# Optimization experiments

Hardware: AMD Instinct MI355X
Metric: run time of the kernel (lower is better)

Reference implementation:

```python
import jax, jax.numpy as jnp
import numpy as np

D_MODEL = 1024
H = 16
D_K = D_MODEL // H
B, S = 1, 4096


def setup_inputs() -> dict:
    key = jax.random.key(0)
    ks = jax.random.split(key, 12)
    std = 1.0 / np.sqrt(D_MODEL)
    inp = {
        "q": jax.random.normal(ks[0], (B, S, D_MODEL), dtype=jnp.float32),
        "k": jax.random.normal(ks[1], (B, S, D_MODEL), dtype=jnp.float32),
        "v": jax.random.normal(ks[2], (B, S, D_MODEL), dtype=jnp.float32),
        "mask": jax.random.randint(ks[3], (B, 1, S, S), 0, 2).astype(bool),
        # nn.Linear params (torch convention: y = x @ W.T + b), weights [out, in]
        "wq": jax.random.uniform(ks[4], (D_MODEL, D_MODEL), jnp.float32, -std, std),
        "bq": jax.random.uniform(ks[5], (D_MODEL,), jnp.float32, -std, std),
        "wk": jax.random.uniform(ks[6], (D_MODEL, D_MODEL), jnp.float32, -std, std),
        "bk": jax.random.uniform(ks[7], (D_MODEL,), jnp.float32, -std, std),
        "wv": jax.random.uniform(ks[8], (D_MODEL, D_MODEL), jnp.float32, -std, std),
        "bv": jax.random.uniform(ks[9], (D_MODEL,), jnp.float32, -std, std),
        "wo": jax.random.uniform(ks[10], (D_MODEL, D_MODEL), jnp.float32, -std, std),
        "bo": jax.random.uniform(ks[11], (D_MODEL,), jnp.float32, -std, std),
    }
    return inp


def _split_heads(x):
    # [b, s, (h d)] -> [b, h, s, d]
    b, s, _ = x.shape
    return x.reshape(b, s, H, D_K).transpose(0, 2, 1, 3)


def reference(q, k, v, mask, wq, bq, wk, bk, wv, bv, wo, bo):
    b, s, d = q.shape
    qh = _split_heads(q @ wq.T + bq)
    kh = _split_heads(k @ wk.T + bk)
    vh = _split_heads(v @ wv.T + bv)
    # NOTE: original scales by sqrt(d_model), not sqrt(d_k) — keep faithful.
    score = jnp.einsum("bhqd,bhkd->bhqk", qh, kh) / jnp.sqrt(jnp.float32(d))
    score = jnp.where(mask, jnp.float32(-1e9), score)
    attn = jax.nn.softmax(score, axis=-1)  # dropout is identity in eval mode
    wv_out = jnp.einsum("bhqk,bhkd->bhqd", attn, vh)
    concat = wv_out.transpose(0, 2, 1, 3).reshape(b, s, d)
    return concat @ wo.T + bo
```

## Files before the change

kernel.cpp:

```cpp
#include <hip/hip_runtime.h>
#include <hip/hip_bf16.h>
#include <math.h>

typedef __attribute__((ext_vector_type(4))) float f32x4;
typedef __attribute__((ext_vector_type(8))) short s16x8;
typedef __attribute__((ext_vector_type(4))) short s16x4;

#define S_LEN 4096
#define DMODEL 1024
#define NHEADS 16
#define DHEAD 64

__device__ __forceinline__ unsigned short f2bf(float f) {
  union { float f; unsigned int u; } x; x.f = f;
  return (unsigned short)((x.u + 0x7FFFu + ((x.u >> 16) & 1u)) >> 16);
}

__device__ __forceinline__ void gload_lds16(const void* g, void* l) {
  __builtin_amdgcn_global_load_lds(
      (const __attribute__((address_space(1))) unsigned int*)g,
      (__attribute__((address_space(3))) unsigned int*)l, 16, 0, 0);
}

__global__ __launch_bounds__(256) void mask_pack(const int* __restrict__ mask,
                                                 unsigned long long* __restrict__ bits) {
  const int qr = blockIdx.x;
  const int wv = threadIdx.x >> 6, l = threadIdx.x & 63;
  const int* row = mask + (size_t)qr * S_LEN;
#pragma unroll
  for (int w0 = 0; w0 < 64; w0 += 4) {
    const int w = w0 + wv;
    unsigned long long b = __ballot(row[w * 64 + l] != 0);
    if (l == 0) bits[(size_t)qr * 64 + w] = b;
  }
}

__global__ __launch_bounds__(256) void cast_bf16(
    const float* __restrict__ s0, const float* __restrict__ s1, const float* __restrict__ s2,
    const float* __restrict__ s3, const float* __restrict__ s4, const float* __restrict__ s5,
    const float* __restrict__ s6, unsigned short* __restrict__ dst) {
  const int z = blockIdx.y;
  const float* src = (z == 0) ? s0 : (z == 1) ? s1 : (z == 2) ? s2 :
                     (z == 3) ? s3 : (z == 4) ? s4 : (z == 5) ? s5 : s6;
  const int n = (z < 3) ? (S_LEN * DMODEL) : (DMODEL * DMODEL);
  unsigned short* d = dst + ((z < 3) ? (size_t)z * S_LEN * DMODEL
                                     : (size_t)3 * S_LEN * DMODEL + (size_t)(z - 3) * DMODEL * DMODEL);
  const int i = (blockIdx.x * 256 + threadIdx.x) * 4;
  if (i < n) {
    f32x4 v = *(const f32x4*)(src + i);
    s16x4 o;
#pragma unroll
    for (int j = 0; j < 4; ++j) o[j] = (short)f2bf(v[j]);
    *(s16x4*)(d + i) = o;
  }
}

template<int A_BF16, int B_BF16, int OUT_MODE>
__device__ __forceinline__ void gemm_body(const void* __restrict__ Ap,
                                          const void* __restrict__ Wp,
                                          const float* __restrict__ bias,
                                          void* __restrict__ outp, float scale) {
  constexpr int K = DMODEL, N = DMODEL, M = S_LEN;
  constexpr int BM = 128, BK = 32, LDT = 40;
  __shared__ unsigned short Alds[BM * LDT];
  __shared__ unsigned short Blds[BM * LDT];
  const int tid = threadIdx.x;
  const int l = tid & 63, wid = tid >> 6;
  const int lr = l & 15, lg = l >> 4;
  const int bm = blockIdx.x * BM;
  const int bn = blockIdx.y * BM;
  const int wm = (wid >> 1) * 64, wn = (wid & 1) * 64;

  f32x4 acc[4][4] = {};

  for (int k0 = 0; k0 < K; k0 += BK) {
    __syncthreads();
    if constexpr (A_BF16) {
      const unsigned short* A = (const unsigned short*)Ap;
      const int col = (tid & 3) * 8, row = tid >> 2;
#pragma unroll
      for (int p = 0; p < 2; ++p) {
        const int r = row + p * 64;
        *(s16x8*)&Alds[r * LDT + col] =
            *(const s16x8*)(A + (size_t)(bm + r) * K + k0 + col);
      }
    } else {
      const float* A = (const float*)Ap;
      const int col = (tid & 7) * 4, row = tid >> 3;
#pragma unroll
      for (int p = 0; p < 4; ++p) {
        const int r = row + p * 32;
        f32x4 vv = *(const f32x4*)(A + (size_t)(bm + r) * K + k0 + col);
        s16x4 o;
#pragma unroll
        for (int j = 0; j < 4; ++j) o[j] = (short)f2bf(vv[j]);
        *(s16x4*)&Alds[r * LDT + col] = o;
      }
    }
    if constexpr (B_BF16) {
      const unsigned short* W = (const unsigned short*)Wp;
      const int col = (tid & 3) * 8, row = tid >> 2;
#pragma unroll
      for (int p = 0; p < 2; ++p) {
        const int r = row + p * 64;
        *(s16x8*)&Blds[r * LDT + col] =
            *(const s16x8*)(W + (size_t)(bn + r) * K + k0 + col);
      }
    } else {
      const float* W = (const float*)Wp;
      const int col = (tid & 7) * 4, row = tid >> 3;
#pragma unroll
      for (int p = 0; p < 4; ++p) {
        const int r = row + p * 32;
        f32x4 vv = *(const f32x4*)(W + (size_t)(bn + r) * K + k0 + col);
        s16x4 o;
#pragma unroll
        for (int j = 0; j < 4; ++j) o[j] = (short)f2bf(vv[j]);
        *(s16x4*)&Blds[r * LDT + col] = o;
      }
    }
    __syncthreads();
    s16x8 af[4], bfr[4];
#pragma unroll
    for (int mi = 0; mi < 4; ++mi)
      af[mi] = *(const s16x8*)&Alds[(wm + mi * 16 + lr) * LDT + lg * 8];
#pragma unroll
    for (int ni = 0; ni < 4; ++ni)
      bfr[ni] = *(const s16x8*)&Blds[(wn + ni * 16 + lr) * LDT + lg * 8];
#pragma unroll
    for (int mi = 0; mi < 4; ++mi)
#pragma unroll
      for (int ni = 0; ni < 4; ++ni)
        acc[mi][ni] = __builtin_amdgcn_mfma_f32_16x16x32_bf16(af[mi], bfr[ni], acc[mi][ni], 0, 0, 0);
  }

#pragma unroll
  for (int ni = 0; ni < 4; ++ni) {
    const int n = bn + wn + ni * 16 + lr;
    const float bv = bias[n];
#pragma unroll
    for (int mi = 0; mi < 4; ++mi) {
#pragma unroll
      for (int j = 0; j < 4; ++j) {
        const int m = bm + wm + mi * 16 + lg * 4 + j;
        const float val = (acc[mi][ni][j] + bv) * scale;
        if constexpr (OUT_MODE == 1) {
          unsigned short* out = (unsigned short*)outp;
          out[((size_t)(n >> 6) * M + m) * DHEAD + (n & 63)] = f2bf(val);
        } else if constexpr (OUT_MODE == 2) {
          unsigned short* out = (unsigned short*)outp;
          out[((size_t)(n >> 6) * DHEAD + (n & 63)) * M + m] = f2bf(val);
        } else {
          float* out = (float*)outp;
          out[(size_t)m * N + n] = val;
        }
      }
    }
  }
}

__global__ __launch_bounds__(256) void proj_qk_f32(
    const float* __restrict__ q, const float* __restrict__ k,
    const float* __restrict__ wq, const float* __restrict__ bq,
    const float* __restrict__ wk, const float* __restrict__ bk,
    unsigned short* __restrict__ ws) {
  const int z = blockIdx.z;
  gemm_body<0, 0, 1>((z == 0) ? q : k, (z == 0) ? wq : wk, (z == 0) ? bq : bk,
                     ws + (size_t)z * S_LEN * DMODEL, (z == 0) ? 0.03125f : 1.0f);
}
__global__ __launch_bounds__(256) void proj_v_f32(
    const float* __restrict__ v, const float* __restrict__ wv,
    const float* __restrict__ bv, unsigned short* __restrict__ out) {
  gemm_body<0, 0, 2>(v, wv, bv, out, 1.0f);
}
__global__ __launch_bounds__(256) void outproj_f32(
    const unsigned short* __restrict__ concat, const float* __restrict__ wo,
    const float* __restrict__ bo, float* __restrict__ out) {
  gemm_body<1, 0, 0>(concat, wo, bo, out, 1.0f);
}

__global__ __launch_bounds__(256) void proj_qk_b16(
    const unsigned short* __restrict__ qb, const unsigned short* __restrict__ kb,
    const unsigned short* __restrict__ wqb, const float* __restrict__ bq,
    const unsigned short* __restrict__ wkb, const float* __restrict__ bk,
    unsigned short* __restrict__ ws) {
  const int z = blockIdx.z;
  gemm_body<1, 1, 1>((z == 0) ? qb : kb, (z == 0) ? wqb : wkb, (z == 0) ? bq : bk,
                     ws + (size_t)z * S_LEN * DMODEL, (z == 0) ? 0.03125f : 1.0f);
}
__global__ __launch_bounds__(256) void proj_v_b16(
    const unsigned short* __restrict__ vb, const unsigned short* __restrict__ wvb,
    const float* __restrict__ bv, unsigned short* __restrict__ out) {
  gemm_body<1, 1, 2>(vb, wvb, bv, out, 1.0f);
}
__global__ __launch_bounds__(256) void outproj_b16(
    const unsigned short* __restrict__ concat, const unsigned short* __restrict__ wob,
    const float* __restrict__ bo, float* __restrict__ out) {
  gemm_body<1, 1, 0>(concat, wob, bo, out, 1.0f);
}

__global__ __launch_bounds__(512, 4) void attn_fwd(
    const unsigned short* __restrict__ Qh, const unsigned short* __restrict__ Kh,
    const unsigned short* __restrict__ Vt, const unsigned long long* __restrict__ bits,
    unsigned short* __restrict__ concat) {
  __shared__ unsigned short Klds[2][64 * 64];
  __shared__ unsigned short Vlds[2][64 * 64];
  __shared__ unsigned short P_lds[8][16][72];

  const int tid = threadIdx.x;
  const int l = tid & 63, wid = tid >> 6;
  const int lr = l & 15, lg = l >> 4;
  const int swz = (blockIdx.x & 7) * 64 + (blockIdx.x >> 3);
  const int h = swz >> 5;
  const int qrow0 = (swz & 31) * 128 + wid * 16;

  const unsigned short* Qbase = Qh + ((size_t)h * S_LEN + qrow0) * DHEAD;
  s16x8 qf[2];
#pragma unroll
  for (int ds = 0; ds < 2; ++ds)
    qf[ds] = *(const s16x8*)(Qbase + lr * DHEAD + ds * 32 + lg * 8);

  const unsigned short* Kbase = Kh + (size_t)h * S_LEN * DHEAD;
  const unsigned short* Vbase = Vt + (size_t)h * DHEAD * S_LEN;
  const unsigned long long* mrow = bits + (size_t)(qrow0 + lr) * 64;

  const int srow = l >> 3;
  const int schunk = (l & 7) ^ srow;
  const unsigned short* Kst = Kbase + (size_t)(wid * 8 + srow) * DHEAD + schunk * 8;
  const unsigned short* Vst = Vbase + (size_t)(wid * 8 + srow) * S_LEN + schunk * 8;
  const int sdst = (wid * 8) * 64;

  f32x4 o_acc[4] = {};
  float lsum = 0.f;

  gload_lds16(Kst, &Klds[0][sdst]);
  gload_lds16(Vst, &Vlds[0][sdst]);
  __syncthreads();

  const int xr = lr & 7;

  for (int t = 0; t < 64; ++t) {
    const int buf = t & 1;
    if (t < 63) {
      gload_lds16(Kst + (size_t)(t + 1) * 64 * DHEAD, &Klds[buf ^ 1][sdst]);
      gload_lds16(Vst + (t + 1) * 64, &Vlds[buf ^ 1][sdst]);
    }

    const unsigned long long mw = mrow[t];

    const unsigned short* Kb = &Klds[buf][0];
    s16x8 kf[8];
#pragma unroll
    for (int kg = 0; kg < 4; ++kg) {
      const int r = kg * 16 + lr;
      kf[kg * 2]     = *(const s16x8*)(Kb + r * 64 + ((lg ^ xr) * 8));
      kf[kg * 2 + 1] = *(const s16x8*)(Kb + r * 64 + (((lg + 4) ^ xr) * 8));
    }
    f32x4 sc[4];
    __builtin_amdgcn_s_setprio(1);
#pragma unroll
    for (int kg = 0; kg < 4; ++kg) {
      f32x4 z = {};
      z = __builtin_amdgcn_mfma_f32_16x16x32_bf16(kf[kg * 2], qf[0], z, 0, 0, 0);
      sc[kg] = __builtin_amdgcn_mfma_f32_16x16x32_bf16(kf[kg * 2 + 1], qf[1], z, 0, 0, 0);
    }
    __builtin_amdgcn_s_setprio(0);

    const unsigned short* Vb = &Vlds[buf][0];
    s16x8 vf[8];
#pragma unroll
    for (int dg = 0; dg < 4; ++dg) {
      const int r = dg * 16 + lr;
      vf[dg * 2]     = *(const s16x8*)(Vb + r * 64 + ((lg ^ xr) * 8));
      vf[dg * 2 + 1] = *(const s16x8*)(Vb + r * 64 + (((lg + 4) ^ xr) * 8));
    }

#pragma unroll
    for (int kg = 0; kg < 4; ++kg) {
      const unsigned int part = (unsigned int)(mw >> (kg * 16 + lg * 4));
#pragma unroll
      for (int j = 0; j < 4; ++j) {
        const float sv = ((part >> j) & 1u) ? -1e9f : sc[kg][j];
        const float p = __expf(sv);
        sc[kg][j] = p;
        lsum += p;
      }
    }

#pragma unroll
    for (int kg = 0; kg < 4; ++kg) {
#pragma unroll
      for (int w = 0; w < 2; ++w) {
        unsigned int pk;
        asm("v_cvt_pk_bf16_f32 %0, %1, %2"
            : "=v"(pk) : "v"(sc[kg][2 * w]), "v"(sc[kg][2 * w + 1]));
        *(unsigned int*)&P_lds[wid][lr][kg * 16 + lg * 4 + 2 * w] = pk;
      }
    }

    s16x8 pf[2];
#pragma unroll
    for (int ks = 0; ks < 2; ++ks)
      pf[ks] = *(const s16x8*)&P_lds[wid][lr][ks * 32 + lg * 8];

    __builtin_amdgcn_s_setprio(1);
#pragma unroll
    for (int dg = 0; dg < 4; ++dg)
#pragma unroll
      for (int ks = 0; ks < 2; ++ks)
        o_acc[dg] = __builtin_amdgcn_mfma_f32_16x16x32_bf16(pf[ks], vf[dg * 2 + ks], o_acc[dg], 0, 0, 0);
    __builtin_amdgcn_s_setprio(0);

    __syncthreads();
  }

  lsum += __shfl_xor(lsum, 16, 64);
  lsum += __shfl_xor(lsum, 32, 64);
  float rs[4];
#pragma unroll
  for (int j = 0; j < 4; ++j) rs[j] = __shfl(lsum, lg * 4 + j, 64);

#pragma unroll
  for (int dg = 0; dg < 4; ++dg)
#pragma unroll
    for (int j = 0; j < 4; ++j) {
      const int qr = qrow0 + lg * 4 + j;
      const int d = dg * 16 + lr;
      concat[(size_t)qr * DMODEL + h * DHEAD + d] = f2bf(o_acc[dg][j] / rs[j]);
    }
}

extern "C" void kernel_launch(void* const* d_in, const int* in_sizes, int n_in,
                              void* d_out, int out_size, void* d_ws, size_t ws_size,
                              hipStream_t stream) {
  const float* q  = (const float*)d_in[0];
  const float* k  = (const float*)d_in[1];
  const float* v  = (const float*)d_in[2];
  const int* mask = (const int*)d_in[3];
  const float* wq = (const float*)d_in[4];
  const float* bq = (const float*)d_in[5];
  const float* wk = (const float*)d_in[6];
  const float* bk = (const float*)d_in[7];
  const float* wv = (const float*)d_in[8];
  const float* bv = (const float*)d_in[9];
  const float* wo = (const float*)d_in[10];
  const float* bo = (const float*)d_in[11];
  float* out = (float*)d_out;

  unsigned short* wsq = (unsigned short*)d_ws;
  unsigned short* wsk = wsq + (size_t)S_LEN * DMODEL;
  unsigned short* wsv = wsk + (size_t)S_LEN * DMODEL;
  unsigned short* wsc = wsv + (size_t)S_LEN * DMODEL;
  unsigned long long* wsbits = (unsigned long long*)(wsc + (size_t)S_LEN * DMODEL);
  unsigned short* cast0 = (unsigned short*)(wsbits + (size_t)S_LEN * 64);
  const size_t need = (size_t)((char*)(cast0 + 3 * (size_t)S_LEN * DMODEL
                                       + 4 * (size_t)DMODEL * DMODEL) - (char*)d_ws);
  const bool big = ws_size >= need;

  mask_pack<<<dim3(S_LEN), dim3(256), 0, stream>>>(mask, wsbits);

  if (big) {
    unsigned short* qb  = cast0;
    unsigned short* kb  = qb + (size_t)S_LEN * DMODEL;
    unsigned short* vb  = kb + (size_t)S_LEN * DMODEL;
    unsigned short* wqb = vb + (size_t)S_LEN * DMODEL;
    unsigned short* wkb = wqb + (size_t)DMODEL * DMODEL;
    unsigned short* wvb = wkb + (size_t)DMODEL * DMODEL;
    unsigned short* wob = wvb + (size_t)DMODEL * DMODEL;
    cast_bf16<<<dim3(4096, 7), dim3(256), 0, stream>>>(q, k, v, wq, wk, wv, wo, qb);
    proj_qk_b16<<<dim3(32, 8, 2), dim3(256), 0, stream>>>(qb, kb, wqb, bq, wkb, bk, wsq);
    proj_v_b16<<<dim3(32, 8), dim3(256), 0, stream>>>(vb, wvb, bv, wsv);
    attn_fwd<<<dim3(512), dim3(512), 0, stream>>>(wsq, wsk, wsv, wsbits, wsc);
    outproj_b16<<<dim3(32, 8), dim3(256), 0, stream>>>(wsc, wob, bo, out);
  } else {
    proj_qk_f32<<<dim3(32, 8, 2), dim3(256), 0, stream>>>(q, k, wq, bq, wk, bk, wsq);
    proj_v_f32<<<dim3(32, 8), dim3(256), 0, stream>>>(v, wv, bv, wsv);
    attn_fwd<<<dim3(512), dim3(512), 0, stream>>>(wsq, wsk, wsv, wsbits, wsc);
    outproj_f32<<<dim3(32, 8), dim3(256), 0, stream>>>(wsc, wo, bo, out);
  }
}
```

Before: 224.7 us.

## Split KV across blocks, double per-wave query rows, and transpose mask to SGPR layout

The attention kernel now processes 32 query rows per wave, so each K/V LDS fragment feeds twice as many MFMAs, and splits the KV range in two across blocks to keep the grid at 512 blocks. A separate combine kernel merges the unnormalised bf16 partial outputs with their row sums. The mask is pre-transposed into per-lane 64-bit words so masking becomes a v_cndmask with an SGPR operand, and exp uses exp2 with log2(e) folded into the Q scale. The Q/K/V projections are merged into one launch. Costs are an extra transpose kernel, a combine kernel, partial-output traffic, and bf16 rounding of the partials before they are combined.

```diff
diff --git a/kernel.cpp b/kernel.cpp
--- a/kernel.cpp
+++ b/kernel.cpp
@@ -14,6 +14,14 @@
 __device__ __forceinline__ unsigned short f2bf(float f) {
   union { float f; unsigned int u; } x; x.f = f;
   return (unsigned short)((x.u + 0x7FFFu + ((x.u >> 16) & 1u)) >> 16);
+}
+
+__device__ __forceinline__ float fexp2(float x) {
+#if __has_builtin(__builtin_amdgcn_exp2f)
+  return __builtin_amdgcn_exp2f(x);
+#else
+  float r; asm("v_exp_f32 %0, %1" : "=v"(r) : "v"(x)); return r;
+#endif
 }
 
 __device__ __forceinline__ void gload_lds16(const void* g, void* l) {
@@ -33,6 +41,22 @@
     unsigned long long b = __ballot(row[w * 64 + l] != 0);
     if (l == 0) bits[(size_t)qr * 64 + w] = b;
   }
+}
+
+__global__ __launch_bounds__(256) void mask_xpose(const unsigned long long* __restrict__ bits,
+                                                  unsigned long long* __restrict__ lmask) {
+  const int wv = blockIdx.x * 4 + (threadIdx.x >> 6);
+  const int l = threadIdx.x & 63, lr = l & 15, lg4 = (l >> 4) * 4;
+  const int qg = wv >> 6, t = wv & 63;
+  const unsigned long long rw = bits[(size_t)(qg * 16 + lr) * 64 + t];
+  unsigned long long mine = 0;
+#pragma unroll
+  for (int w = 0; w < 16; ++w) {
+    const int sh = (w >> 2) * 16 + (w & 3) + lg4;
+    unsigned long long b = __ballot(((rw >> sh) & 1ull) != 0);
+    if (l == w) mine = b;
+  }
+  if (l < 16) lmask[((size_t)qg * 64 + t) * 16 + l] = mine;
 }
 
 __global__ __launch_bounds__(256) void cast_bf16(
@@ -159,19 +183,35 @@
   }
 }
 
-__global__ __launch_bounds__(256) void proj_qk_f32(
-    const float* __restrict__ q, const float* __restrict__ k,
+#define QSCALE 0.04508422f
+
+__global__ __launch_bounds__(256) void proj_qkv_b16(
+    const unsigned short* __restrict__ qb, const unsigned short* __restrict__ kb,
+    const unsigned short* __restrict__ vb,
+    const unsigned short* __restrict__ wqb, const float* __restrict__ bq,
+    const unsigned short* __restrict__ wkb, const float* __restrict__ bk,
+    const unsigned short* __restrict__ wvb, const float* __restrict__ bv,
+    unsigned short* __restrict__ ws) {
+  const int z = blockIdx.z;
+  if (z == 0)      gemm_body<1, 1, 1>(qb, wqb, bq, ws, QSCALE);
+  else if (z == 1) gemm_body<1, 1, 1>(kb, wkb, bk, ws + (size_t)S_LEN * DMODEL, 1.0f);
+  else             gemm_body<1, 1, 2>(vb, wvb, bv, ws + (size_t)2 * S_LEN * DMODEL, 1.0f);
+}
+__global__ __launch_bounds__(256) void proj_qkv_f32(
+    const float* __restrict__ q, const float* __restrict__ k, const float* __restrict__ v,
     const float* __restrict__ wq, const float* __restrict__ bq,
     const float* __restrict__ wk, const float* __restrict__ bk,
+    const float* __restrict__ wv, const float* __restrict__ bv,
     unsigned short* __restrict__ ws) {
   const int z = blockIdx.z;
-  gemm_body<0, 0, 1>((z == 0) ? q : k, (z == 0) ? wq : wk, (z == 0) ? bq : bk,
-                     ws + (size_t)z * S_LEN * DMODEL, (z == 0) ? 0.03125f : 1.0f);
-}
-__global__ __launch_bounds__(256) void proj_v_f32(
-    const float* __restrict__ v, const float* __restrict__ wv,
-    const float* __restrict__ bv, unsigned short* __restrict__ out) {
-  gemm_body<0, 0, 2>(v, wv, bv, out, 1.0f);
+  if (z == 0)      gemm_body<0, 0, 1>(q, wq, bq, ws, QSCALE);
+  else if (z == 1) gemm_body<0, 0, 1>(k, wk, bk, ws + (size_t)S_LEN * DMODEL, 1.0f);
+  else             gemm_body<0, 0, 2>(v, wv, bv, ws + (size_t)2 * S_LEN * DMODEL, 1.0f);
+}
+__global__ __launch_bounds__(256) void outproj_b16(
+    const unsigned short* __restrict__ concat, const unsigned short* __restrict__ wob,
+    const float* __restrict__ bo, float* __restrict__ out) {
+  gemm_body<1, 1, 0>(concat, wob, bo, out, 1.0f);
 }
 __global__ __launch_bounds__(256) void outproj_f32(
     const unsigned short* __restrict__ concat, const float* __restrict__ wo,
@@ -179,59 +219,52 @@
   gemm_body<1, 0, 0>(concat, wo, bo, out, 1.0f);
 }
 
-__global__ __launch_bounds__(256) void proj_qk_b16(
-    const unsigned short* __restrict__ qb, const unsigned short* __restrict__ kb,
-    const unsigned short* __restrict__ wqb, const float* __restrict__ bq,
-    const unsigned short* __restrict__ wkb, const float* __restrict__ bk,
-    unsigned short* __restrict__ ws) {
-  const int z = blockIdx.z;
-  gemm_body<1, 1, 1>((z == 0) ? qb : kb, (z == 0) ? wqb : wkb, (z == 0) ? bq : bk,
-                     ws + (size_t)z * S_LEN * DMODEL, (z == 0) ? 0.03125f : 1.0f);
-}
-__global__ __launch_bounds__(256) void proj_v_b16(
-    const unsigned short* __restrict__ vb, const unsigned short* __restrict__ wvb,
-    const float* __restrict__ bv, unsigned short* __restrict__ out) {
-  gemm_body<1, 1, 2>(vb, wvb, bv, out, 1.0f);
-}
-__global__ __launch_bounds__(256) void outproj_b16(
-    const unsigned short* __restrict__ concat, const unsigned short* __restrict__ wob,
-    const float* __restrict__ bo, float* __restrict__ out) {
-  gemm_body<1, 1, 0>(concat, wob, bo, out, 1.0f);
-}
-
+template<int NSPLIT>
 __global__ __launch_bounds__(512, 4) void attn_fwd(
     const unsigned short* __restrict__ Qh, const unsigned short* __restrict__ Kh,
-    const unsigned short* __restrict__ Vt, const unsigned long long* __restrict__ bits,
-    unsigned short* __restrict__ concat) {
+    const unsigned short* __restrict__ Vt, const unsigned long long* __restrict__ lmask,
+    unsigned short* __restrict__ outp,
+    float* __restrict__ lpart) {
   __shared__ unsigned short Klds[2][64 * 64];
   __shared__ unsigned short Vlds[2][64 * 64];
-  __shared__ unsigned short P_lds[8][16][72];
+  __shared__ unsigned short P_lds[8][32][72];
 
   const int tid = threadIdx.x;
   const int l = tid & 63, wid = tid >> 6;
   const int lr = l & 15, lg = l >> 4;
-  const int swz = (blockIdx.x & 7) * 64 + (blockIdx.x >> 3);
-  const int h = swz >> 5;
-  const int qrow0 = (swz & 31) * 128 + wid * 16;
+  const int per = 32 * NSPLIT;
+  const int swz = (blockIdx.x & 7) * per + (blockIdx.x >> 3);
+  const int h = swz / (16 * NSPLIT);
+  const int split = (NSPLIT == 2) ? ((swz >> 4) & 1) : 0;
+  const int qb = swz & 15;
+  const int qrow0 = qb * 256 + wid * 32;
+  const int kv0 = split * (S_LEN / NSPLIT);
+  constexpr int NT = (S_LEN / NSPLIT) / 64;
+  const int T0 = kv0 >> 6;
 
   const unsigned short* Qbase = Qh + ((size_t)h * S_LEN + qrow0) * DHEAD;
-  s16x8 qf[2];
-#pragma unroll
-  for (int ds = 0; ds < 2; ++ds)
-    qf[ds] = *(const s16x8*)(Qbase + lr * DHEAD + ds * 32 + lg * 8);
-
-  const unsigned short* Kbase = Kh + (size_t)h * S_LEN * DHEAD;
-  const unsigned short* Vbase = Vt + (size_t)h * DHEAD * S_LEN;
-  const unsigned long long* mrow = bits + (size_t)(qrow0 + lr) * 64;
+  s16x8 qf[2][2];
+#pragma unroll
+  for (int sub = 0; sub < 2; ++sub)
+#pragma unroll
+    for (int ds = 0; ds < 2; ++ds)
+      qf[sub][ds] = *(const s16x8*)(Qbase + (sub * 16 + lr) * DHEAD + ds * 32 + lg * 8);
+
+  const int wid_u = __builtin_amdgcn_readfirstlane(wid);
+  const int qg0 = qb * 16 + wid_u * 2;
+  const unsigned long long* mq0 = lmask + (size_t)qg0 * 64 * 16;
+  const unsigned long long* mq1 = mq0 + (size_t)64 * 16;
 
   const int srow = l >> 3;
   const int schunk = (l & 7) ^ srow;
-  const unsigned short* Kst = Kbase + (size_t)(wid * 8 + srow) * DHEAD + schunk * 8;
-  const unsigned short* Vst = Vbase + (size_t)(wid * 8 + srow) * S_LEN + schunk * 8;
+  const unsigned short* Kst = Kh + (size_t)h * S_LEN * DHEAD
+                              + (size_t)(kv0 + wid * 8 + srow) * DHEAD + schunk * 8;
+  const unsigned short* Vst = Vt + (size_t)h * DHEAD * S_LEN
+                              + (size_t)(wid * 8 + srow) * S_LEN + kv0 + schunk * 8;
   const int sdst = (wid * 8) * 64;
 
-  f32x4 o_acc[4] = {};
-  float lsum = 0.f;
+  f32x4 o_acc[2][4] = {};
+  float lsum[2] = {0.f, 0.f};
 
   gload_lds16(Kst, &Klds[0][sdst]);
   gload_lds16(Vst, &Vlds[0][sdst]);
@@ -239,95 +272,144 @@
 
   const int xr = lr & 7;
 
-  for (int t = 0; t < 64; ++t) {
+  for (int t = 0; t < NT; ++t) {
     const int buf = t & 1;
-    if (t < 63) {
+    if (t < NT - 1) {
       gload_lds16(Kst + (size_t)(t + 1) * 64 * DHEAD, &Klds[buf ^ 1][sdst]);
       gload_lds16(Vst + (t + 1) * 64, &Vlds[buf ^ 1][sdst]);
     }
 
-    const unsigned long long mw = mrow[t];
-
     const unsigned short* Kb = &Klds[buf][0];
-    s16x8 kf[8];
+    f32x4 sc[2][4];
+    __builtin_amdgcn_s_setprio(1);
 #pragma unroll
     for (int kg = 0; kg < 4; ++kg) {
       const int r = kg * 16 + lr;
-      kf[kg * 2]     = *(const s16x8*)(Kb + r * 64 + ((lg ^ xr) * 8));
-      kf[kg * 2 + 1] = *(const s16x8*)(Kb + r * 64 + (((lg + 4) ^ xr) * 8));
-    }
-    f32x4 sc[4];
+      s16x8 k0 = *(const s16x8*)(Kb + r * 64 + ((lg ^ xr) * 8));
+      s16x8 k1 = *(const s16x8*)(Kb + r * 64 + (((lg + 4) ^ xr) * 8));
+#pragma unroll
+      for (int sub = 0; sub < 2; ++sub) {
+        f32x4 z = {};
+        z = __builtin_amdgcn_mfma_f32_16x16x32_bf16(k0, qf[sub][0], z, 0, 0, 0);
+        sc[sub][kg] = __builtin_amdgcn_mfma_f32_16x16x32_bf16(k1, qf[sub][1], z, 0, 0, 0);
+      }
+    }
+    __builtin_amdgcn_s_setprio(0);
+
+    const size_t mo = (size_t)(T0 + t) * 16;
+#pragma unroll
+    for (int sub = 0; sub < 2; ++sub) {
+      const unsigned long long* qp = (sub ? mq1 : mq0) + mo;
+#pragma unroll
+      for (int kg = 0; kg < 4; ++kg) {
+        float p[4];
+#pragma unroll
+        for (int j = 0; j < 4; ++j) {
+          const unsigned long long mw = qp[kg * 4 + j];
+          float pv = fexp2(sc[sub][kg][j]);
+          asm("v_cndmask_b32 %0, %1, 0, %2" : "=v"(pv) : "v"(pv), "s"(mw));
+          p[j] = pv;
+          lsum[sub] += pv;
+        }
+        unsigned int w0, w1;
+        asm("v_cvt_pk_bf16_f32 %0, %1, %2" : "=v"(w0) : "v"(p[0]), "v"(p[1]));
+        asm("v_cvt_pk_bf16_f32 %0, %1, %2" : "=v"(w1) : "v"(p[2]), "v"(p[3]));
+        uint2 pk; pk.x = w0; pk.y = w1;
+        *(uint2*)&P_lds[wid][sub * 16 + lr][kg * 16 + lg * 4] = pk;
+      }
+    }
+    asm volatile("s_waitcnt lgkmcnt(0)" ::: "memory");
+    __builtin_amdgcn_sched_barrier(0);
+
+    s16x8 pf[2][2];
+#pragma unroll
+    for (int sub = 0; sub < 2; ++sub)
+#pragma unroll
+      for (int ks = 0; ks < 2; ++ks)
+        pf[sub][ks] = *(const s16x8*)&P_lds[wid][sub * 16 + lr][ks * 32 + lg * 8];
+
+    const unsigned short* Vb = &Vlds[buf][0];
     __builtin_amdgcn_s_setprio(1);
-#pragma unroll
-    for (int kg = 0; kg < 4; ++kg) {
-      f32x4 z = {};
-      z = __builtin_amdgcn_mfma_f32_16x16x32_bf16(kf[kg * 2], qf[0], z, 0, 0, 0);
-      sc[kg] = __builtin_amdgcn_mfma_f32_16x16x32_bf16(kf[kg * 2 + 1], qf[1], z, 0, 0, 0);
-    }
-    __builtin_amdgcn_s_setprio(0);
-
-    const unsigned short* Vb = &Vlds[buf][0];
-    s16x8 vf[8];
 #pragma unroll
     for (int dg = 0; dg < 4; ++dg) {
       const int r = dg * 16 + lr;
-      vf[dg * 2]     = *(const s16x8*)(Vb + r * 64 + ((lg ^ xr) * 8));
-      vf[dg * 2 + 1] = *(const s16x8*)(Vb + r * 64 + (((lg + 4) ^ xr) * 8));
-    }
-
-#pragma unroll
-    for (int kg = 0; kg < 4; ++kg) {
-      const unsigned int part = (unsigned int)(mw >> (kg * 16 + lg * 4));
-#pragma unroll
-      for (int j = 0; j < 4; ++j) {
-        const float sv = ((part >> j) & 1u) ? -1e9f : sc[kg][j];
-        const float p = __expf(sv);
-        sc[kg][j] = p;
-        lsum += p;
-      }
-    }
-
-#pragma unroll
-    for (int kg = 0; kg < 4; ++kg) {
-#pragma unroll
-      for (int w = 0; w < 2; ++w) {
-        unsigned int pk;
-        asm("v_cvt_pk_bf16_f32 %0, %1, %2"
-            : "=v"(pk) : "v"(sc[kg][2 * w]), "v"(sc[kg][2 * w + 1]));
-        *(unsigned int*)&P_lds[wid][lr][kg * 16 + lg * 4 + 2 * w] = pk;
-      }
-    }
-
-    s16x8 pf[2];
-#pragma unroll
-    for (int ks = 0; ks < 2; ++ks)
-      pf[ks] = *(const s16x8*)&P_lds[wid][lr][ks * 32 + lg * 8];
-
-    __builtin_amdgcn_s_setprio(1);
-#pragma unroll
-    for (int dg = 0; dg < 4; ++dg)
-#pragma unroll
-      for (int ks = 0; ks < 2; ++ks)
-        o_acc[dg] = __builtin_amdgcn_mfma_f32_16x16x32_bf16(pf[ks], vf[dg * 2 + ks], o_acc[dg], 0, 0, 0);
+      s16x8 v0 = *(const s16x8*)(Vb + r * 64 + ((lg ^ xr) * 8));
+      s16x8 v1 = *(const s16x8*)(Vb + r * 64 + (((lg + 4) ^ xr) * 8));
+#pragma unroll
+      for (int sub = 0; sub < 2; ++sub) {
+        o_acc[sub][dg] = __builtin_amdgcn_mfma_f32_16x16x32_bf16(pf[sub][0], v0, o_acc[sub][dg], 0, 0, 0);
+        o_acc[sub][dg] = __builtin_amdgcn_mfma_f32_16x16x32_bf16(pf[sub][1], v1, o_acc[sub][dg], 0, 0, 0);
+      }
+    }
     __builtin_amdgcn_s_setprio(0);
 
     __syncthreads();
   }
 
-  lsum += __shfl_xor(lsum, 16, 64);
-  lsum += __shfl_xor(lsum, 32, 64);
-  float rs[4];
-#pragma unroll
-  for (int j = 0; j < 4; ++j) rs[j] = __shfl(lsum, lg * 4 + j, 64);
-
-#pragma unroll
-  for (int dg = 0; dg < 4; ++dg)
-#pragma unroll
-    for (int j = 0; j < 4; ++j) {
-      const int qr = qrow0 + lg * 4 + j;
-      const int d = dg * 16 + lr;
-      concat[(size_t)qr * DMODEL + h * DHEAD + d] = f2bf(o_acc[dg][j] / rs[j]);
-    }
+#pragma unroll
+  for (int sub = 0; sub < 2; ++sub) {
+    lsum[sub] += __shfl_xor(lsum[sub], 16, 64);
+    lsum[sub] += __shfl_xor(lsum[sub], 32, 64);
+  }
+
+  if constexpr (NSPLIT == 2) {
+    unsigned short* op = outp + ((size_t)(split * NHEADS + h) * S_LEN) * DHEAD;
+#pragma unroll
+    for (int sub = 0; sub < 2; ++sub)
+#pragma unroll
+      for (int dg = 0; dg < 4; ++dg)
+#pragma unroll
+        for (int j = 0; j < 4; ++j) {
+          const int q = qrow0 + sub * 16 + lg * 4 + j;
+          op[(size_t)q * DHEAD + dg * 16 + lr] = f2bf(o_acc[sub][dg][j]);
+        }
+    if (l < 16) {
+      float* lp = lpart + (size_t)(split * NHEADS + h) * S_LEN + qrow0;
+      lp[lr] = lsum[0];
+      lp[16 + lr] = lsum[1];
+    }
+  } else {
+    float rs[2][4];
+#pragma unroll
+    for (int sub = 0; sub < 2; ++sub)
+#pragma unroll
+      for (int j = 0; j < 4; ++j)
+        rs[sub][j] = __shfl(lsum[sub], lg * 4 + j, 64);
+#pragma unroll
+    for (int sub = 0; sub < 2; ++sub)
+#pragma unroll
+      for (int dg = 0; dg < 4; ++dg)
+#pragma unroll
+        for (int j = 0; j < 4; ++j) {
+          const int q = qrow0 + sub * 16 + lg * 4 + j;
+          outp[(size_t)q * DMODEL + h * DHEAD + dg * 16 + lr] =
+              f2bf(o_acc[sub][dg][j] / rs[sub][j]);
+        }
+  }
+}
+
+__global__ __launch_bounds__(256) void attn_combine(
+    const unsigned short* __restrict__ opart, const float* __restrict__ lpart,
+    unsigned short* __restrict__ concat) {
+  const int idx = blockIdx.x * 256 + threadIdx.x;
+  const int d4 = (idx & 15) * 4;
+  const int hq = idx >> 4;
+  const int h = hq >> 12, q = hq & 4095;
+  const size_t o0 = ((size_t)h * S_LEN + q) * DHEAD + d4;
+  const size_t o1 = o0 + (size_t)NHEADS * S_LEN * DHEAD;
+  const float linv = 1.0f / (lpart[(size_t)h * S_LEN + q] +
+                             lpart[(size_t)(NHEADS + h) * S_LEN + q]);
+  s16x4 a = *(const s16x4*)(opart + o0);
+  s16x4 b = *(const s16x4*)(opart + o1);
+  s16x4 r;
+#pragma unroll
+  for (int i = 0; i < 4; ++i) {
+    union { unsigned int u; float f; } xa, xb;
+    xa.u = ((unsigned int)(unsigned short)a[i]) << 16;
+    xb.u = ((unsigned int)(unsigned short)b[i]) << 16;
+    r[i] = (short)f2bf((xa.f + xb.f) * linv);
+  }
+  *(s16x4*)(concat + ((size_t)q * DMODEL + h * DHEAD + d4)) = r;
 }
 
 extern "C" void kernel_launch(void* const* d_in, const int* in_sizes, int n_in,
@@ -347,35 +429,36 @@
   const float* bo = (const float*)d_in[11];
   float* out = (float*)d_out;
 
+  const size_t SD = (size_t)S_LEN * DMODEL, DD = (size_t)DMODEL * DMODEL;
   unsigned short* wsq = (unsigned short*)d_ws;
-  unsigned short* wsk = wsq + (size_t)S_LEN * DMODEL;
-  unsigned short* wsv = wsk + (size_t)S_LEN * DMODEL;
-  unsigned short* wsc = wsv + (size_t)S_LEN * DMODEL;
-  unsigned long long* wsbits = (unsigned long long*)(wsc + (size_t)S_LEN * DMODEL);
-  unsigned short* cast0 = (unsigned short*)(wsbits + (size_t)S_LEN * 64);
-  const size_t need = (size_t)((char*)(cast0 + 3 * (size_t)S_LEN * DMODEL
-                                       + 4 * (size_t)DMODEL * DMODEL) - (char*)d_ws);
+  unsigned short* wsc = wsq + 3 * SD;
+  unsigned long long* wsbits = (unsigned long long*)(wsc + SD);
+  unsigned long long* wslm = wsbits + (size_t)S_LEN * 64;
+  unsigned short* cast0 = (unsigned short*)(wslm + (size_t)256 * 64 * 16);
+  const size_t need = (size_t)((char*)(cast0 + 3 * SD + 4 * DD) - (char*)d_ws);
   const bool big = ws_size >= need;
 
   mask_pack<<<dim3(S_LEN), dim3(256), 0, stream>>>(mask, wsbits);
+  mask_xpose<<<dim3(4096), dim3(256), 0, stream>>>(wsbits, wslm);
 
   if (big) {
     unsigned short* qb  = cast0;
-    unsigned short* kb  = qb + (size_t)S_LEN * DMODEL;
-    unsigned short* vb  = kb + (size_t)S_LEN * DMODEL;
-    unsigned short* wqb = vb + (size_t)S_LEN * DMODEL;
-    unsigned short* wkb = wqb + (size_t)DMODEL * DMODEL;
-    unsigned short* wvb = wkb + (size_t)DMODEL * DMODEL;
-    unsigned short* wob = wvb + (size_t)DMODEL * DMODEL;
-    cast_bf16<<<dim3(4096, 7), dim3(256), 0, stream>>>(q, k, v, wq, wk, wv, wo, qb);
-    proj_qk_b16<<<dim3(32, 8, 2), dim3(256), 0, stream>>>(qb, kb, wqb, bq, wkb, bk, wsq);
-    proj_v_b16<<<dim3(32, 8), dim3(256), 0, stream>>>(vb, wvb, bv, wsv);
-    attn_fwd<<<dim3(512), dim3(512), 0, stream>>>(wsq, wsk, wsv, wsbits, wsc);
+    unsigned short* kb  = qb + SD;
+    unsigned short* vb  = kb + SD;
+    unsigned short* wqb = vb + SD;
+    unsigned short* wkb = wqb + DD;
+    unsigned short* wvb = wkb + DD;
+    unsigned short* wob = wvb + DD;
+    unsigned short* opart = cast0;
+    float* lpart = (float*)vb;
+    cast_bf16<<<dim3(4096, 7), dim3(256), 0, stream>>>(q, k, v, wq, wk, wv, wo, cast0);
+    proj_qkv_b16<<<dim3(32, 8, 3), dim3(256), 0, stream>>>(qb, kb, vb, wqb, bq, wkb, bk, wvb, bv, wsq);
+    attn_fwd<2><<<dim3(512), dim3(512), 0, stream>>>(wsq, wsq + SD, wsq + 2 * SD, wslm, opart, lpart);
+    attn_combine<<<dim3(4096), dim3(256), 0, stream>>>(opart, lpart, wsc);
     outproj_b16<<<dim3(32, 8), dim3(256), 0, stream>>>(wsc, wob, bo, out);
   } else {
-    proj_qk_f32<<<dim3(32, 8, 2), dim3(256), 0, stream>>>(q, k, wq, bq, wk, bk, wsq);
-    proj_v_f32<<<dim3(32, 8), dim3(256), 0, stream>>>(v, wv, bv, wsv);
-    attn_fwd<<<dim3(512), dim3(512), 0, stream>>>(wsq, wsk, wsv, wsbits, wsc);
+    proj_qkv_f32<<<dim3(32, 8, 3), dim3(256), 0, stream>>>(q, k, v, wq, bq, wk, bk, wv, bv, wsq);
+    attn_fwd<1><<<dim3(256), dim3(512), 0, stream>>>(wsq, wsq + SD, wsq + 2 * SD, wslm, wsc, nullptr);
     outproj_f32<<<dim3(32, 8), dim3(256), 0, stream>>>(wsc, wo, bo, out);
   }
 }
```

New measurement: 199.1 us. 1.13x faster.
